# Kernel tuning notes

Hardware: AMD Instinct MI355X
Metric: run time of the kernel (lower is better)

## Reference

```python
import jax, jax.numpy as jnp
import numpy as np

N_NODES = 100000
N_EDGES = 3200000
NFEAT = 512
DIMS = [NFEAT, 12, 10, 8, 6, 4, 16]  # layer widths; 16 = nout


def setup_inputs() -> dict:
    key = jax.random.key(0)
    ks = jax.random.split(key, 16)
    inp = {
        "x": jax.random.normal(ks[0], (N_NODES, NFEAT), dtype=jnp.float32),
        "edge_index": jax.random.randint(ks[1], (2, N_EDGES), 0, N_NODES, dtype=jnp.int32),
        "edge_weight": jax.random.uniform(ks[2], (N_EDGES,), dtype=jnp.float32) * (1.0 / 32.0),
    }
    # GCN layer params: support = x @ W; out = adj @ support + b
    for i in range(6):
        fan_in, fan_out = DIMS[i], DIMS[i + 1]
        scale = 1.0 / np.sqrt(fan_in)
        inp[f"W{i+1}"] = jax.random.uniform(ks[3 + 2 * i], (fan_in, fan_out), dtype=jnp.float32, minval=-scale, maxval=scale)
        inp[f"b{i+1}"] = jax.random.uniform(ks[4 + 2 * i], (fan_out,), dtype=jnp.float32, minval=-scale, maxval=scale)
    return inp


def _gcn_layer(h, src, dst, w, W, b):
    # support = h @ W  -> [N, out]; out = A @ support + b via edge scatter-add
    support = h @ W
    msgs = w[:, None] * support[src]            # [E, out]
    agg = jax.ops.segment_sum(msgs, dst, num_segments=N_NODES)
    return agg + b


def reference(x, edge_index, edge_weight, W1, b1, W2, b2, W3, b3, W4, b4, W5, b5, W6, b6):
    src, dst = edge_index[0], edge_index[1]
    # Eval-mode forward: F.dropout(training=False) is identity.
    h = x
    for W, b in ((W1, b1), (W2, b2), (W3, b3), (W4, b4), (W5, b5), (W6, b6)):
        h = _gcn_layer(h, src, dst, edge_weight, W, b)
    return h
```

## Files before the change

kernel.cpp:

```cpp
#include <hip/hip_runtime.h>
#include <hip/hip_fp16.h>

constexpr int NF = 512;
constexpr int SCAN_B = 1024;
constexpr int DPB = 256;
constexpr int CHUNK = 16384;
constexpr int BMAX = 9216;
constexpr float WSCALE = 1048544.0f;
constexpr float WINV = 1.0f / 1048544.0f;

__device__ __forceinline__ float dot16(const float* a, const float* w, float acc) {
#pragma unroll
  for (int j = 0; j < 16; ++j) acc = fmaf(a[j], w[j], acc);
  return acc;
}

template <int COUT>
__global__ __launch_bounds__(256) void gemm_big_count_kernel(
    const float* __restrict__ x, const float* __restrict__ W,
    __half* __restrict__ sup, int n, const int* __restrict__ ei,
    int* __restrict__ cnt, int E, int nbuck, int nch) {
  __shared__ __align__(16) float sW[COUT * NF];
  __shared__ __align__(16) float part[4][COUT][64];
  if ((int)blockIdx.x < nch) {
    int* hist = (int*)sW;
    const int c = blockIdx.x;
    for (int b = threadIdx.x; b < nbuck; b += 256) hist[b] = 0;
    __syncthreads();
    const int base = c * CHUNK;
    for (int i = threadIdx.x; i < CHUNK; i += 256) {
      const int e = base + i;
      if (e < E) atomicAdd(&hist[ei[E + e] >> 8], 1);
    }
    __syncthreads();
    for (int b = threadIdx.x; b < nbuck; b += 256) cnt[b * nch + c] = hist[b];
    return;
  }

  for (int i = threadIdx.x; i < COUT * NF; i += 256) {
    int c = i / NF, k = i - c * NF;
    sW[c * NF + k] = W[(size_t)k * COUT + c];
  }
  __syncthreads();

  const int w = threadIdx.x >> 6;
  const int lane = threadIdx.x & 63;
  const int vbase = (blockIdx.x - nch) * 64;
  const int v = vbase + lane;
  const int ve = (v < n) ? v : (n - 1);

  float acc[COUT];
#pragma unroll
  for (int c = 0; c < COUT; ++c) acc[c] = 0.f;

  const float4* xr = (const float4*)(x + (size_t)ve * NF) + w * 32;
  float4 cur[4], nxt[4];
#pragma unroll
  for (int j = 0; j < 4; ++j) cur[j] = xr[j];
  for (int kb = 0; kb < 8; ++kb) {
    const int kn = (kb + 1 < 8) ? kb + 1 : kb;
#pragma unroll
    for (int j = 0; j < 4; ++j) nxt[j] = xr[kn * 4 + j];
    const float* af = (const float*)cur;
    const int kq = w * 8 + kb;
#pragma unroll
    for (int c = 0; c < COUT; ++c) {
      const float4* wr = (const float4*)(&sW[c * NF + kq * 16]);
      float4 wq[4];
#pragma unroll
      for (int j = 0; j < 4; ++j) wq[j] = wr[j];
      acc[c] = dot16(af, (const float*)wq, acc[c]);
    }
#pragma unroll
    for (int j = 0; j < 4; ++j) cur[j] = nxt[j];
  }

#pragma unroll
  for (int c = 0; c < COUT; ++c) part[w][c][lane] = acc[c];
  __syncthreads();

  if (w == 0 && v < n) {
    float r[COUT];
#pragma unroll
    for (int c = 0; c < COUT; ++c)
      r[c] = part[0][c][lane] + part[1][c][lane] + part[2][c][lane] +
             part[3][c][lane];
    union { uint4 u; __half2 h[4]; } o1;
    union { uint2 u; __half2 h[2]; } o2;
#pragma unroll
    for (int g = 0; g < 4; ++g) o1.h[g] = __floats2half2_rn(r[2 * g], r[2 * g + 1]);
#pragma unroll
    for (int g = 0; g < 2; ++g) o2.h[g] = __floats2half2_rn(r[8 + 2 * g], r[9 + 2 * g]);
    __half* o = sup + (size_t)v * 16;
    *(uint4*)o = o1.u;
    *(uint2*)(o + 8) = o2.u;
  }
}


__global__ __launch_bounds__(256) void scan1_kernel(const int* __restrict__ src,
                                                    int* __restrict__ dst,
                                                    int* __restrict__ bsums, int m) {
  __shared__ int s[256];
  const int t = threadIdx.x;
  const int idx = blockIdx.x * SCAN_B + t * 4;
  int4 d = {0, 0, 0, 0};
  if (idx + 3 < m) {
    d = *(const int4*)(src + idx);
  } else {
    if (idx + 0 < m) d.x = src[idx + 0];
    if (idx + 1 < m) d.y = src[idx + 1];
    if (idx + 2 < m) d.z = src[idx + 2];
    if (idx + 3 < m) d.w = src[idx + 3];
  }
  const int sum = d.x + d.y + d.z + d.w;
  s[t] = sum;
  __syncthreads();
  for (int off = 1; off < 256; off <<= 1) {
    int val = (t >= off) ? s[t - off] : 0;
    __syncthreads();
    s[t] += val;
    __syncthreads();
  }
  const int excl = s[t] - sum;
  if (t == 255) bsums[blockIdx.x] = s[255];
  if (idx + 0 < m) dst[idx + 0] = excl;
  if (idx + 1 < m) dst[idx + 1] = excl + d.x;
  if (idx + 2 < m) dst[idx + 2] = excl + d.x + d.y;
  if (idx + 3 < m) dst[idx + 3] = excl + d.x + d.y + d.z;
}

__global__ __launch_bounds__(256) void scan2_kernel(const int* __restrict__ bsums,
                                                    int* __restrict__ bscan, int nb) {
  __shared__ int s[256];
  const int t = threadIdx.x;
  const int v = (t < nb) ? bsums[t] : 0;
  s[t] = v;
  __syncthreads();
  for (int off = 1; off < 256; off <<= 1) {
    int val = (t >= off) ? s[t - off] : 0;
    __syncthreads();
    s[t] += val;
    __syncthreads();
  }
  if (t < nb) bscan[t] = s[t] - v;
}

__global__ __launch_bounds__(256) void scatterC_kernel(
    const int* __restrict__ ei, const float* __restrict__ ew,
    const int* __restrict__ offsp, const int* __restrict__ bscan,
    int2* __restrict__ pairs, int E, int nbuck, int nch) {
  __shared__ int cur[512];
  const int c = blockIdx.x;
  for (int b = threadIdx.x; b < nbuck; b += 256) {
    const int idx = b * nch + c;
    cur[b] = offsp[idx] + bscan[idx >> 10];
  }
  __syncthreads();
  const int base = c * CHUNK;
  for (int i = threadIdx.x; i < CHUNK; i += 256) {
    const int e = base + i;
    if (e >= E) break;
    const int s = ei[e];
    const int d = ei[E + e];
    const float w = ew[e];
    const int pos = atomicAdd(&cur[d >> 8], 1);
    pairs[pos] = make_int2(s | ((d & (DPB - 1)) << 17), __float_as_int(w));
  }
}

__global__ __launch_bounds__(256) void bucketD_kernel(
    const int* __restrict__ offsp, const int* __restrict__ bscan,
    const int2* __restrict__ pairs, unsigned* __restrict__ cpairs,
    int* __restrict__ rowptr, int n, int E, int nbuck, int nch) {
  __shared__ unsigned stage[BMAX];
  __shared__ int h[DPB];
  __shared__ int s[DPB];
  __shared__ int cur[DPB];
  const int b = blockIdx.x;
  const int t = threadIdx.x;
  if (b == 0 && t == 0) rowptr[n] = E;
  const int i0 = b * nch;
  const int base = offsp[i0] + bscan[i0 >> 10];
  int end;
  if (b + 1 < nbuck) {
    const int i1 = (b + 1) * nch;
    end = offsp[i1] + bscan[i1 >> 10];
  } else {
    end = E;
  }
  const int cnt = end - base;

  for (int i = t; i < DPB; i += 256) h[i] = 0;
  __syncthreads();
  for (int i = t; i < cnt; i += 256) {
    const int2 p = pairs[base + i];
    atomicAdd(&h[(p.x >> 17) & (DPB - 1)], 1);
  }
  __syncthreads();
  const int own = h[t];
  s[t] = own;
  __syncthreads();
  for (int off = 1; off < 256; off <<= 1) {
    int val = (t >= off) ? s[t - off] : 0;
    __syncthreads();
    s[t] += val;
    __syncthreads();
  }
  const int excl = s[t] - own;
  cur[t] = excl;
  const int dst = b * DPB + t;
  if (dst < n) rowptr[dst] = base + excl;
  __syncthreads();
  for (int i = t; i < cnt; i += 256) {
    const int2 p = pairs[base + i];
    const int r = atomicAdd(&cur[(p.x >> 17) & (DPB - 1)], 1);
    const float w = __int_as_float(p.y);
    const unsigned wq = (unsigned)__float2int_rn(w * WSCALE);
    if (r < BMAX) stage[r] = (unsigned)(p.x & 0x1FFFF) | (wq << 17);
  }
  __syncthreads();
  const int lim = cnt < BMAX ? cnt : BMAX;
  for (int i = t; i < lim; i += 256) cpairs[base + i] = stage[i];
}


template <int PIN, int CIN>
__device__ __forceinline__ void load_row_h(const __half* __restrict__ sup,
                                           unsigned p, float* hv, float* wout) {
  *wout = (float)(p >> 17) * WINV;
  const __half* hr = sup + (size_t)(p & 0x1FFFF) * PIN;
  __half2 h[6];
  if constexpr (PIN == 16) {
    union { uint4 u; __half2 h[4]; } a;
    union { uint2 u; __half2 h[2]; } b;
    a.u = *(const uint4*)hr;
    b.u = *(const uint2*)(hr + 8);
    h[0] = a.h[0]; h[1] = a.h[1]; h[2] = a.h[2]; h[3] = a.h[3];
    h[4] = b.h[0]; h[5] = b.h[1];
  } else if constexpr (PIN == 8) {
    union { uint4 u; __half2 h[4]; } a;
    a.u = *(const uint4*)hr;
    h[0] = a.h[0]; h[1] = a.h[1]; h[2] = a.h[2]; h[3] = a.h[3];
  } else {
    union { uint2 u; __half2 h[2]; } a;
    a.u = *(const uint2*)hr;
    h[0] = a.h[0]; h[1] = a.h[1];
  }
#pragma unroll
  for (int g = 0; g < CIN / 2; ++g) {
    float2 f = __half22float2(h[g]);
    hv[2 * g] = f.x;
    hv[2 * g + 1] = f.y;
  }
}

template <int PIN, int CIN, int COUT, int POUT, bool AGG_BIAS, bool OUT_BIAS,
          bool IDENT, typename TOUT>
__global__ __launch_bounds__(256) void pull_one_kernel(
    const int* __restrict__ rowptr, const unsigned* __restrict__ cp,
    const __half* __restrict__ sup, const float* __restrict__ bagg,
    const float* __restrict__ W, const float* __restrict__ bout,
    TOUT* __restrict__ outp, int n) {
  __shared__ float sW[IDENT ? 1 : CIN * 16];
  __shared__ float sba[16];
  __shared__ float sbo[16];
  const int tt = threadIdx.x;
  if constexpr (!IDENT) {
    for (int i = tt; i < CIN * 16; i += 256) {
      const int k = i >> 4, j = i & 15;
      sW[i] = (j < COUT) ? W[k * COUT + j] : 0.f;
    }
  }
  if constexpr (AGG_BIAS)
    if (tt < CIN) sba[tt] = bagg[tt];
  if constexpr (OUT_BIAS)
    if (tt < COUT) sbo[tt] = bout[tt];
  __syncthreads();

  const int gt = blockIdx.x * 256 + tt;
  const int v = gt >> 3;
  const int lane = gt & 7;
  if (v >= n) return;
  const int beg = rowptr[v];
  const int end = rowptr[v + 1];

  float acc[CIN];
#pragma unroll
  for (int c = 0; c < CIN; ++c) acc[c] = 0.f;

  int i = beg + lane;
  for (; i + 8 < end; i += 16) {
    const unsigned p0 = cp[i];
    const unsigned p1 = cp[i + 8];
    float w0, w1, h0[CIN], h1[CIN];
    load_row_h<PIN, CIN>(sup, p0, h0, &w0);
    load_row_h<PIN, CIN>(sup, p1, h1, &w1);
#pragma unroll
    for (int c = 0; c < CIN; ++c) acc[c] = fmaf(w0, h0[c], acc[c]);
#pragma unroll
    for (int c = 0; c < CIN; ++c) acc[c] = fmaf(w1, h1[c], acc[c]);
  }
  if (i < end) {
    const unsigned p0 = cp[i];
    float w0, h0[CIN];
    load_row_h<PIN, CIN>(sup, p0, h0, &w0);
#pragma unroll
    for (int c = 0; c < CIN; ++c) acc[c] = fmaf(w0, h0[c], acc[c]);
  }

#pragma unroll
  for (int c = 0; c < CIN; ++c) {
    acc[c] += __shfl_xor(acc[c], 1);
    acc[c] += __shfl_xor(acc[c], 2);
    acc[c] += __shfl_xor(acc[c], 4);
    if constexpr (AGG_BIAS) acc[c] += sba[c];
  }

  if constexpr (IDENT) {
    if (lane == 0) {
      union { uint2 u; __half2 h[2]; } o;
      o.h[0] = __floats2half2_rn(acc[0], acc[1]);
      o.h[1] = __floats2half2_rn(acc[2], acc[3]);
      *(uint2*)((__half*)outp + (size_t)v * POUT) = o.u;
    }
  } else {
    if (lane * 4 < POUT) {
      const int col = lane * 4;
      float r[4];
#pragma unroll
      for (int j = 0; j < 4; ++j) {
        float a = OUT_BIAS ? sbo[col + j] : 0.f;
#pragma unroll
        for (int k = 0; k < CIN; ++k) a = fmaf(acc[k], sW[k * 16 + col + j], a);
        r[j] = a;
      }
      if constexpr (sizeof(TOUT) == 2) {
        union { uint2 u; __half2 h[2]; } o;
        o.h[0] = __floats2half2_rn(r[0], r[1]);
        o.h[1] = __floats2half2_rn(r[2], r[3]);
        *(uint2*)((__half*)outp + (size_t)v * POUT + col) = o.u;
      } else {
        float4 o;
        o.x = r[0]; o.y = r[1]; o.z = r[2]; o.w = r[3];
        *(float4*)((float*)outp + (size_t)v * POUT + col) = o;
      }
    }
  }
}

extern "C" void kernel_launch(void* const* d_in, const int* in_sizes, int n_in,
                              void* d_out, int out_size, void* d_ws,
                              size_t ws_size, hipStream_t stream) {
  const float* x = (const float*)d_in[0];
  const int* ei = (const int*)d_in[1];
  const float* ew = (const float*)d_in[2];
  const float* W1 = (const float*)d_in[3];
  const float* b1 = (const float*)d_in[4];
  const float* W2 = (const float*)d_in[5];
  const float* b2 = (const float*)d_in[6];
  const float* W3 = (const float*)d_in[7];
  const float* b3 = (const float*)d_in[8];
  const float* W4 = (const float*)d_in[9];
  const float* b4 = (const float*)d_in[10];
  const float* W5 = (const float*)d_in[11];
  const float* b5 = (const float*)d_in[12];
  const float* W6 = (const float*)d_in[13];
  const float* b6 = (const float*)d_in[14];
  float* out = (float*)d_out;

  const int n = in_sizes[0] / NF;
  const int E = in_sizes[2];

  const int nbuck = (n + DPB - 1) / DPB;
  const int nch = (E + CHUNK - 1) / CHUNK;
  const int M = nbuck * nch;
  const int Mpad = (M + 3) & ~3;

  __half* A = (__half*)d_ws;
  __half* B = A + (size_t)n * 16;
  int* cnt = (int*)(B + (size_t)n * 16);
  int* offs = cnt + Mpad;
  int* bsums = offs + Mpad;
  int* bscan = bsums + 256;
  int* rowptr = bscan + 256;
  uintptr_t up = (uintptr_t)(rowptr + n + 1);
  up = (up + 15) & ~(uintptr_t)15;
  unsigned* cpairs = (unsigned*)up;
  int2* pairs = (int2*)(cpairs + E);

  const int gnb = (n + 63) / 64;
  const int nsb = (M + SCAN_B - 1) / SCAN_B;
  const int gq8 = (n * 8 + 255) / 256;

  gemm_big_count_kernel<12>
      <<<nch + gnb, 256, 0, stream>>>(x, W1, A, n, ei, cnt, E, nbuck, nch);
  scan1_kernel<<<nsb, 256, 0, stream>>>(cnt, offs, bsums, M);
  scan2_kernel<<<1, 256, 0, stream>>>(bsums, bscan, nsb);
  scatterC_kernel<<<nch, 256, 0, stream>>>(ei, ew, offs, bscan, pairs, E, nbuck, nch);
  bucketD_kernel<<<nbuck, 256, 0, stream>>>(offs, bscan, pairs, cpairs, rowptr,
                                            n, E, nbuck, nch);

  pull_one_kernel<16, 12, 10, 16, true, false, false, __half>
      <<<gq8, 256, 0, stream>>>(rowptr, cpairs, A, b1, W2, nullptr, B, n);
  pull_one_kernel<16, 10, 8, 8, true, false, false, __half>
      <<<gq8, 256, 0, stream>>>(rowptr, cpairs, B, b2, W3, nullptr, A, n);
  pull_one_kernel<8, 8, 6, 8, true, false, false, __half>
      <<<gq8, 256, 0, stream>>>(rowptr, cpairs, A, b3, W4, nullptr, B, n);
  pull_one_kernel<8, 6, 4, 4, true, false, false, __half>
      <<<gq8, 256, 0, stream>>>(rowptr, cpairs, B, b4, W5, nullptr, A, n);
  pull_one_kernel<4, 4, 4, 4, true, false, true, __half>
      <<<gq8, 256, 0, stream>>>(rowptr, cpairs, A, b5, nullptr, nullptr, B, n);
  pull_one_kernel<4, 4, 16, 16, false, true, false, float>
      <<<gq8, 256, 0, stream>>>(rowptr, cpairs, B, nullptr, W6, b6, out, n);
}
```

Measured before the change: 261.9 us.

## Fuse block-sum scan into consumers and co-schedule GEMM with edge scatter

Removes the single-block scan2 kernel by having each scatter block and each bucketD block redundantly scan the block sums in shared memory. The dense layer-1 GEMM is moved out of the count kernel and merged with the scatter pass, so the GEMM and the scatter run in one launch and the count kernel becomes a light standalone launch. This saves one launch and aims to overlap the bandwidth-heavy GEMM with the atomic-heavy scatter. The cost is a repeated 256-wide scan in every scatter and bucket block.

After: 279.3 us. +6.7%, slower.

```diff
diff --git a/kernel.cpp b/kernel.cpp
--- a/kernel.cpp
+++ b/kernel.cpp
@@ -15,88 +15,21 @@
   return acc;
 }
 
-template <int COUT>
-__global__ __launch_bounds__(256) void gemm_big_count_kernel(
-    const float* __restrict__ x, const float* __restrict__ W,
-    __half* __restrict__ sup, int n, const int* __restrict__ ei,
-    int* __restrict__ cnt, int E, int nbuck, int nch) {
-  __shared__ __align__(16) float sW[COUT * NF];
-  __shared__ __align__(16) float part[4][COUT][64];
-  if ((int)blockIdx.x < nch) {
-    int* hist = (int*)sW;
-    const int c = blockIdx.x;
-    for (int b = threadIdx.x; b < nbuck; b += 256) hist[b] = 0;
-    __syncthreads();
-    const int base = c * CHUNK;
-    for (int i = threadIdx.x; i < CHUNK; i += 256) {
-      const int e = base + i;
-      if (e < E) atomicAdd(&hist[ei[E + e] >> 8], 1);
-    }
-    __syncthreads();
-    for (int b = threadIdx.x; b < nbuck; b += 256) cnt[b * nch + c] = hist[b];
-    return;
-  }
-
-  for (int i = threadIdx.x; i < COUT * NF; i += 256) {
-    int c = i / NF, k = i - c * NF;
-    sW[c * NF + k] = W[(size_t)k * COUT + c];
-  }
-  __syncthreads();
-
-  const int w = threadIdx.x >> 6;
-  const int lane = threadIdx.x & 63;
-  const int vbase = (blockIdx.x - nch) * 64;
-  const int v = vbase + lane;
-  const int ve = (v < n) ? v : (n - 1);
-
-  float acc[COUT];
-#pragma unroll
-  for (int c = 0; c < COUT; ++c) acc[c] = 0.f;
-
-  const float4* xr = (const float4*)(x + (size_t)ve * NF) + w * 32;
-  float4 cur[4], nxt[4];
-#pragma unroll
-  for (int j = 0; j < 4; ++j) cur[j] = xr[j];
-  for (int kb = 0; kb < 8; ++kb) {
-    const int kn = (kb + 1 < 8) ? kb + 1 : kb;
-#pragma unroll
-    for (int j = 0; j < 4; ++j) nxt[j] = xr[kn * 4 + j];
-    const float* af = (const float*)cur;
-    const int kq = w * 8 + kb;
-#pragma unroll
-    for (int c = 0; c < COUT; ++c) {
-      const float4* wr = (const float4*)(&sW[c * NF + kq * 16]);
-      float4 wq[4];
-#pragma unroll
-      for (int j = 0; j < 4; ++j) wq[j] = wr[j];
-      acc[c] = dot16(af, (const float*)wq, acc[c]);
-    }
-#pragma unroll
-    for (int j = 0; j < 4; ++j) cur[j] = nxt[j];
-  }
-
-#pragma unroll
-  for (int c = 0; c < COUT; ++c) part[w][c][lane] = acc[c];
-  __syncthreads();
-
-  if (w == 0 && v < n) {
-    float r[COUT];
-#pragma unroll
-    for (int c = 0; c < COUT; ++c)
-      r[c] = part[0][c][lane] + part[1][c][lane] + part[2][c][lane] +
-             part[3][c][lane];
-    union { uint4 u; __half2 h[4]; } o1;
-    union { uint2 u; __half2 h[2]; } o2;
-#pragma unroll
-    for (int g = 0; g < 4; ++g) o1.h[g] = __floats2half2_rn(r[2 * g], r[2 * g + 1]);
-#pragma unroll
-    for (int g = 0; g < 2; ++g) o2.h[g] = __floats2half2_rn(r[8 + 2 * g], r[9 + 2 * g]);
-    __half* o = sup + (size_t)v * 16;
-    *(uint4*)o = o1.u;
-    *(uint2*)(o + 8) = o2.u;
-  }
-}
-
+__global__ __launch_bounds__(256) void countA_kernel(const int* __restrict__ ei,
+                                                     int* __restrict__ cnt, int E,
+                                                     int nbuck, int nch) {
+  __shared__ int hist[512];
+  const int c = blockIdx.x;
+  for (int b = threadIdx.x; b < nbuck; b += 256) hist[b] = 0;
+  __syncthreads();
+  const int base = c * CHUNK;
+  for (int i = threadIdx.x; i < CHUNK; i += 256) {
+    const int e = base + i;
+    if (e < E) atomicAdd(&hist[ei[E + e] >> 8], 1);
+  }
+  __syncthreads();
+  for (int b = threadIdx.x; b < nbuck; b += 256) cnt[b * nch + c] = hist[b];
+}
 
 __global__ __launch_bounds__(256) void scan1_kernel(const int* __restrict__ src,
                                                     int* __restrict__ dst,
@@ -130,47 +63,113 @@
   if (idx + 3 < m) dst[idx + 3] = excl + d.x + d.y + d.z;
 }
 
-__global__ __launch_bounds__(256) void scan2_kernel(const int* __restrict__ bsums,
-                                                    int* __restrict__ bscan, int nb) {
-  __shared__ int s[256];
+template <int COUT>
+__global__ __launch_bounds__(256) void gemm_scatter_kernel(
+    const float* __restrict__ x, const float* __restrict__ W,
+    __half* __restrict__ sup, int n, const int* __restrict__ ei,
+    const float* __restrict__ ew, const int* __restrict__ offsp,
+    const int* __restrict__ bsums, int nsb, int2* __restrict__ pairs, int E,
+    int nbuck, int nch, int gnb) {
+  __shared__ __align__(16) float sW[COUT * NF];
+  __shared__ __align__(16) float part[4][COUT][64];
   const int t = threadIdx.x;
-  const int v = (t < nb) ? bsums[t] : 0;
-  s[t] = v;
-  __syncthreads();
-  for (int off = 1; off < 256; off <<= 1) {
-    int val = (t >= off) ? s[t - off] : 0;
-    __syncthreads();
-    s[t] += val;
-    __syncthreads();
-  }
-  if (t < nb) bscan[t] = s[t] - v;
-}
-
-__global__ __launch_bounds__(256) void scatterC_kernel(
-    const int* __restrict__ ei, const float* __restrict__ ew,
-    const int* __restrict__ offsp, const int* __restrict__ bscan,
-    int2* __restrict__ pairs, int E, int nbuck, int nch) {
-  __shared__ int cur[512];
-  const int c = blockIdx.x;
-  for (int b = threadIdx.x; b < nbuck; b += 256) {
-    const int idx = b * nch + c;
-    cur[b] = offsp[idx] + bscan[idx >> 10];
-  }
-  __syncthreads();
-  const int base = c * CHUNK;
-  for (int i = threadIdx.x; i < CHUNK; i += 256) {
-    const int e = base + i;
-    if (e >= E) break;
-    const int s = ei[e];
-    const int d = ei[E + e];
-    const float w = ew[e];
-    const int pos = atomicAdd(&cur[d >> 8], 1);
-    pairs[pos] = make_int2(s | ((d & (DPB - 1)) << 17), __float_as_int(w));
+
+  if ((int)blockIdx.x >= gnb) {
+    int* sb = (int*)sW;
+    int* cur = (int*)part;
+    const int v = (t < nsb) ? bsums[t] : 0;
+    sb[t] = v;
+    __syncthreads();
+    for (int off = 1; off < 256; off <<= 1) {
+      int val = (t >= off) ? sb[t - off] : 0;
+      __syncthreads();
+      sb[t] += val;
+      __syncthreads();
+    }
+    const int incl = sb[t];
+    __syncthreads();
+    sb[t] = incl - v;
+    __syncthreads();
+    const int c = blockIdx.x - gnb;
+    for (int b = t; b < nbuck; b += 256) {
+      const int idx = b * nch + c;
+      cur[b] = offsp[idx] + sb[idx >> 10];
+    }
+    __syncthreads();
+    const int base = c * CHUNK;
+    for (int i = t; i < CHUNK; i += 256) {
+      const int e = base + i;
+      if (e >= E) break;
+      const int s = ei[e];
+      const int d = ei[E + e];
+      const float w = ew[e];
+      const int pos = atomicAdd(&cur[d >> 8], 1);
+      pairs[pos] = make_int2(s | ((d & (DPB - 1)) << 17), __float_as_int(w));
+    }
+    return;
+  }
+
+  for (int i = t; i < COUT * NF; i += 256) {
+    int c = i / NF, k = i - c * NF;
+    sW[c * NF + k] = W[(size_t)k * COUT + c];
+  }
+  __syncthreads();
+
+  const int w = t >> 6;
+  const int lane = t & 63;
+  const int v = blockIdx.x * 64 + lane;
+  const int ve = (v < n) ? v : (n - 1);
+
+  float acc[COUT];
+#pragma unroll
+  for (int c = 0; c < COUT; ++c) acc[c] = 0.f;
+
+  const float4* xr = (const float4*)(x + (size_t)ve * NF) + w * 32;
+  float4 cur4[4], nxt[4];
+#pragma unroll
+  for (int j = 0; j < 4; ++j) cur4[j] = xr[j];
+  for (int kb = 0; kb < 8; ++kb) {
+    const int kn = (kb + 1 < 8) ? kb + 1 : kb;
+#pragma unroll
+    for (int j = 0; j < 4; ++j) nxt[j] = xr[kn * 4 + j];
+    const float* af = (const float*)cur4;
+    const int kq = w * 8 + kb;
+#pragma unroll
+    for (int c = 0; c < COUT; ++c) {
+      const float4* wr = (const float4*)(&sW[c * NF + kq * 16]);
+      float4 wq[4];
+#pragma unroll
+      for (int j = 0; j < 4; ++j) wq[j] = wr[j];
+      acc[c] = dot16(af, (const float*)wq, acc[c]);
+    }
+#pragma unroll
+    for (int j = 0; j < 4; ++j) cur4[j] = nxt[j];
+  }
+
+#pragma unroll
+  for (int c = 0; c < COUT; ++c) part[w][c][lane] = acc[c];
+  __syncthreads();
+
+  if (w == 0 && v < n) {
+    float r[COUT];
+#pragma unroll
+    for (int c = 0; c < COUT; ++c)
+      r[c] = part[0][c][lane] + part[1][c][lane] + part[2][c][lane] +
+             part[3][c][lane];
+    union { uint4 u; __half2 h[4]; } o1;
+    union { uint2 u; __half2 h[2]; } o2;
+#pragma unroll
+    for (int g = 0; g < 4; ++g) o1.h[g] = __floats2half2_rn(r[2 * g], r[2 * g + 1]);
+#pragma unroll
+    for (int g = 0; g < 2; ++g) o2.h[g] = __floats2half2_rn(r[8 + 2 * g], r[9 + 2 * g]);
+    __half* o = sup + (size_t)v * 16;
+    *(uint4*)o = o1.u;
+    *(uint2*)(o + 8) = o2.u;
   }
 }
 
 __global__ __launch_bounds__(256) void bucketD_kernel(
-    const int* __restrict__ offsp, const int* __restrict__ bscan,
+    const int* __restrict__ offsp, const int* __restrict__ bsums, int nsb,
     const int2* __restrict__ pairs, unsigned* __restrict__ cpairs,
     int* __restrict__ rowptr, int n, int E, int nbuck, int nch) {
   __shared__ unsigned stage[BMAX];
@@ -180,16 +179,33 @@
   const int b = blockIdx.x;
   const int t = threadIdx.x;
   if (b == 0 && t == 0) rowptr[n] = E;
+
+  {
+    const int v = (t < nsb) ? bsums[t] : 0;
+    s[t] = v;
+    __syncthreads();
+    for (int off = 1; off < 256; off <<= 1) {
+      int val = (t >= off) ? s[t - off] : 0;
+      __syncthreads();
+      s[t] += val;
+      __syncthreads();
+    }
+    const int incl = s[t];
+    __syncthreads();
+    s[t] = incl - v;
+    __syncthreads();
+  }
   const int i0 = b * nch;
-  const int base = offsp[i0] + bscan[i0 >> 10];
+  const int base = offsp[i0] + s[i0 >> 10];
   int end;
   if (b + 1 < nbuck) {
     const int i1 = (b + 1) * nch;
-    end = offsp[i1] + bscan[i1 >> 10];
+    end = offsp[i1] + s[i1 >> 10];
   } else {
     end = E;
   }
   const int cnt = end - base;
+  __syncthreads();
 
   for (int i = t; i < DPB; i += 256) h[i] = 0;
   __syncthreads();
@@ -382,8 +398,7 @@
   int* cnt = (int*)(B + (size_t)n * 16);
   int* offs = cnt + Mpad;
   int* bsums = offs + Mpad;
-  int* bscan = bsums + 256;
-  int* rowptr = bscan + 256;
+  int* rowptr = bsums + 256;
   uintptr_t up = (uintptr_t)(rowptr + n + 1);
   up = (up + 15) & ~(uintptr_t)15;
   unsigned* cpairs = (unsigned*)up;
@@ -393,13 +408,12 @@
   const int nsb = (M + SCAN_B - 1) / SCAN_B;
   const int gq8 = (n * 8 + 255) / 256;
 
-  gemm_big_count_kernel<12>
-      <<<nch + gnb, 256, 0, stream>>>(x, W1, A, n, ei, cnt, E, nbuck, nch);
+  countA_kernel<<<nch, 256, 0, stream>>>(ei, cnt, E, nbuck, nch);
   scan1_kernel<<<nsb, 256, 0, stream>>>(cnt, offs, bsums, M);
-  scan2_kernel<<<1, 256, 0, stream>>>(bsums, bscan, nsb);
-  scatterC_kernel<<<nch, 256, 0, stream>>>(ei, ew, offs, bscan, pairs, E, nbuck, nch);
-  bucketD_kernel<<<nbuck, 256, 0, stream>>>(offs, bscan, pairs, cpairs, rowptr,
-                                            n, E, nbuck, nch);
+  gemm_scatter_kernel<12><<<gnb + nch, 256, 0, stream>>>(
+      x, W1, A, n, ei, ew, offs, bsums, nsb, pairs, E, nbuck, nch, gnb);
+  bucketD_kernel<<<nbuck, 256, 0, stream>>>(offs, bsums, nsb, pairs, cpairs,
+                                            rowptr, n, E, nbuck, nch);
 
   pull_one_kernel<16, 12, 10, 16, true, false, false, __half>
       <<<gq8, 256, 0, stream>>>(rowptr, cpairs, A, b1, W2, nullptr, B, n);
```
